# Kernel optimization log

Measured on AMD Instinct MI355X. Metric: run time of the kernel, lower is better.

Reference implementation:

```python
import jax, jax.numpy as jnp
import numpy as np

L, D, H, B, SX, SY, VS, VT = 6, 1024, 16, 4, 512, 512, 32000, 32000
DK = D // H
FF = 4 * D
EPS = 1e-3          # LayerNorm eps (added to std, not var)
SCALE_EMB = float(np.sqrt(D))
NEG = -1e30         # stands in for -inf; fully-masked rows are zeroed after softmax


def pos_encoding(length, d):
    # tensor2tensor-style sinusoid: [sin | cos] concatenated along channels
    nt = d // 2
    lti = np.log(1e4) / (nt - 1)
    inv = np.exp(np.arange(nt) * -lti)
    st = np.arange(length)[:, None] * inv[None, :]
    return jnp.asarray(np.concatenate([np.sin(st), np.cos(st)], axis=1), jnp.float32)


def layer_norm(z, a, b):
    # faithful to the torch module: uses unbiased std (ddof=1) and divides by (std + eps)
    mu = z.mean(-1, keepdims=True)
    sig = jnp.sqrt(((z - mu) ** 2).sum(-1, keepdims=True) / (z.shape[-1] - 1))
    return (z - mu) / (sig + EPS) * a + b


def mha(xq, xkv, wq, wk, wv, wo, mask):
    # xq: (b, lq, D), xkv: (b, lk, D); head-chunking of channel dim == reshape to (H, DK)
    b, lq, _ = xq.shape
    q = (xq @ wq.T).reshape(b, lq, H, DK)
    k = (xkv @ wk.T).reshape(b, -1, H, DK)
    v = (xkv @ wv.T).reshape(b, -1, H, DK)
    s = jnp.einsum('bqhd,bkhd->bhqk', q, k) * (1.0 / np.sqrt(DK))
    m = mask[:, None, :, :]
    s = jnp.where(m, s, NEG)
    att = jax.nn.softmax(s, axis=-1)
    att = att * m.any(-1, keepdims=True)  # replicates NaN->0 for fully masked rows
    c = jnp.einsum('bhqk,bkhd->bqhd', att, v).reshape(b, lq, D)
    return c @ wo.T


def setup_inputs():
    key = jax.random.key(0)
    ks = jax.random.split(key, 10)
    s = 0.02
    emb_x = (jax.random.normal(ks[0], (VS, D), jnp.float32) * s).at[0].set(0.0)  # padding_idx=0
    emb_y = (jax.random.normal(ks[1], (VT, D), jnp.float32) * s).at[0].set(0.0)
    return {
        'emb_x': emb_x, 'emb_y': emb_y,
        'enc_qkvo': jax.random.normal(ks[2], (L, 4, D, D), jnp.float32) * s,
        'enc_ln_s': jnp.ones((L, 2, D), jnp.float32), 'enc_ln_b': jnp.zeros((L, 2, D), jnp.float32),
        'enc_w1': jax.random.normal(ks[3], (L, FF, D), jnp.float32) * s, 'enc_b1': jnp.zeros((L, FF), jnp.float32),
        'enc_w2': jax.random.normal(ks[4], (L, D, FF), jnp.float32) * s, 'enc_b2': jnp.zeros((L, D), jnp.float32),
        'dec_qkvo': jax.random.normal(ks[5], (L, 8, D, D), jnp.float32) * s,
        'dec_ln_s': jnp.ones((L, 3, D), jnp.float32), 'dec_ln_b': jnp.zeros((L, 3, D), jnp.float32),
        'dec_w1': jax.random.normal(ks[6], (L, FF, D), jnp.float32) * s, 'dec_b1': jnp.zeros((L, FF), jnp.float32),
        'dec_w2': jax.random.normal(ks[7], (L, D, FF), jnp.float32) * s, 'dec_b2': jnp.zeros((L, D), jnp.float32),
        'x_block': jax.random.randint(ks[8], (B, SX), 0, VS),
        'y_block': jax.random.randint(ks[9], (B, SY), 0, VT),
    }


def reference(emb_x, emb_y, enc_qkvo, enc_ln_s, enc_ln_b, enc_w1, enc_b1, enc_w2, enc_b2,
              dec_qkvo, dec_ln_s, dec_ln_b, dec_w1, dec_b1, dec_w2, dec_b2, x_block, y_block):
    # internal layout (b, len, D); torch code uses (b, D, len) -- math is identical
    ex = emb_x[x_block] * SCALE_EMB + pos_encoding(SX, D)[None]
    ey = emb_y[y_block] * SCALE_EMB + pos_encoding(SY, D)[None]
    xv = x_block != 0
    yv = y_block != 0
    xx = xv[:, :, None] & xv[:, None, :]                                   # (B, qx, kx)
    xy = yv[:, :, None] & xv[:, None, :]                                   # (B, qy, kx)
    yy = (yv[:, :, None] & yv[:, None, :]) & jnp.tril(jnp.ones((SY, SY), bool))[None]
    e = ex
    for i in range(L):
        sub = mha(e, e, enc_qkvo[i, 0], enc_qkvo[i, 1], enc_qkvo[i, 2], enc_qkvo[i, 3], xx)
        e = layer_norm(e + sub, enc_ln_s[i, 0], enc_ln_b[i, 0])
        sub = jax.nn.relu(e @ enc_w1[i].T + enc_b1[i]) @ enc_w2[i].T + enc_b2[i]
        e = layer_norm(e + sub, enc_ln_s[i, 1], enc_ln_b[i, 1])
    z = e
    e = ey
    for i in range(L):
        sub = mha(e, e, dec_qkvo[i, 0], dec_qkvo[i, 1], dec_qkvo[i, 2], dec_qkvo[i, 3], yy)
        e = layer_norm(e + sub, dec_ln_s[i, 0], dec_ln_b[i, 0])
        sub = mha(e, z, dec_qkvo[i, 4], dec_qkvo[i, 5], dec_qkvo[i, 6], dec_qkvo[i, 7], xy)
        e = layer_norm(e + sub, dec_ln_s[i, 1], dec_ln_b[i, 1])
        sub = jax.nn.relu(e @ dec_w1[i].T + dec_b1[i]) @ dec_w2[i].T + dec_b2[i]
        e = layer_norm(e + sub, dec_ln_s[i, 2], dec_ln_b[i, 2])
    return e @ emb_y.T  # tied output projection -> (B, SY, VT)
```

## Files before the change

### kernel.cpp

```cpp
#include <hip/hip_runtime.h>

typedef unsigned short u16;
typedef float f32x4 __attribute__((ext_vector_type(4)));
typedef __bf16 bf16x8 __attribute__((ext_vector_type(8)));
typedef u16 u16x8 __attribute__((ext_vector_type(8)));

#define DEV __device__ __forceinline__

DEV u16 f2bf(float f) {
  unsigned u = __builtin_bit_cast(unsigned, f);
  u += 0x7fffu + ((u >> 16) & 1u);
  return (u16)(u >> 16);
}

DEV float wsum(float v) {
#pragma unroll
  for (int o = 32; o > 0; o >>= 1) v += __shfl_xor(v, o, 64);
  return v;
}
DEV float gmax16(float v) {
#pragma unroll
  for (int o = 8; o > 0; o >>= 1) v = fmaxf(v, __shfl_xor(v, o, 64));
  return v;
}
DEV float gsum16(float v) {
#pragma unroll
  for (int o = 8; o > 0; o >>= 1) v += __shfl_xor(v, o, 64);
  return v;
}

DEV void gld16(const void* g, void* l) {
  __builtin_amdgcn_global_load_lds((const __attribute__((address_space(1))) void*)g,
                                   (__attribute__((address_space(3))) void*)l, 16, 0, 0);
}

DEV void remap_bxy(int& bx, int& by) {
  const int gx = gridDim.x, gy = gridDim.y;
  const int flat = blockIdx.y * gx + blockIdx.x;
  const int nwg = gx * gy;
  const int q = nwg >> 3, r = nwg & 7;
  const int xcd = flat & 7, li = flat >> 3;
  const int wg = (xcd < r ? xcd * (q + 1) : r * (q + 1) + (xcd - r) * q) + li;
  by = wg % gy;
  bx = wg / gy;
}

template <int BM, int BN, int MODE>
__global__ __launch_bounds__(256, 2) void gemm_k(
    const u16* __restrict__ A, const u16* __restrict__ B, int lda, int ldb, int K,
    float alpha, const float* __restrict__ bias, float* __restrict__ Cf, int ldc,
    u16* __restrict__ Cb, u16* __restrict__ qp, u16* __restrict__ kp,
    u16* __restrict__ vp, int n_off) {
  constexpr int FM = BM / 32, FN = BN / 32;
  constexpr int CHA = BM / 8, CHT = (BM + BN) / 8;
  __shared__ u16 lds[2][(BM + BN) * 64];
  const int lane = threadIdx.x & 63, wid = threadIdx.x >> 6;
  const int wr = wid >> 1, wc = wid & 1;
  int bx, by;
  remap_bxy(bx, by);
  const u16* gA = A + (long)(by * BM) * lda;
  const u16* gB = B + (long)(bx * BN) * ldb;

  const f32x4 zero4 = {0.f, 0.f, 0.f, 0.f};
  f32x4 acc[FM][FN];
#pragma unroll
  for (int m = 0; m < FM; ++m)
#pragma unroll
    for (int n = 0; n < FN; ++n) acc[m][n] = zero4;

  const int r8 = lane >> 3, sl = lane & 7;

  auto stage = [&](int buf, int kt) {
    const int kb = kt << 6;
#pragma unroll
    for (int c0 = 0; c0 < CHT; c0 += 4) {
      const int c = c0 + wid;
      u16* l = &lds[buf][c << 9];
      const u16* g;
      if (c < CHA) {
        int r = (c << 3) + r8;
        g = gA + (long)r * lda + kb + ((sl ^ (r & 7)) << 3);
      } else {
        int r = ((c - CHA) << 3) + r8;
        g = gB + (long)r * ldb + kb + ((sl ^ (r & 7)) << 3);
      }
      gld16(g, l);
    }
  };

  const int KT = K >> 6;
  stage(0, 0);
  __syncthreads();
  int cur = 0;
  for (int kt = 0; kt < KT; ++kt) {
    if (kt + 1 < KT) stage(cur ^ 1, kt + 1);
    const u16* lA = &lds[cur][0];
    const u16* lB = &lds[cur][BM << 6];
#pragma unroll
    for (int kk = 0; kk < 2; ++kk) {
      bf16x8 af[FM], bv[FN];
#pragma unroll
      for (int m = 0; m < FM; ++m) {
        int r = wr * (BM / 2) + m * 16 + (lane & 15);
        int slot = ((kk << 2) | (lane >> 4)) ^ (r & 7);
        af[m] = *(const bf16x8*)(lA + (r << 6) + (slot << 3));
      }
#pragma unroll
      for (int n = 0; n < FN; ++n) {
        int r = wc * (BN / 2) + n * 16 + (lane & 15);
        int slot = ((kk << 2) | (lane >> 4)) ^ (r & 7);
        bv[n] = *(const bf16x8*)(lB + (r << 6) + (slot << 3));
      }
#pragma unroll
      for (int m = 0; m < FM; ++m)
#pragma unroll
        for (int n = 0; n < FN; ++n)
          acc[m][n] = __builtin_amdgcn_mfma_f32_16x16x32_bf16(af[m], bv[n], acc[m][n], 0, 0, 0);
    }
    __syncthreads();
    cur ^= 1;
  }

  const int rb = by * BM + wr * (BM / 2) + ((lane >> 4) << 2);
  const int cb = bx * BN + wc * (BN / 2) + (lane & 15);
#pragma unroll
  for (int m = 0; m < FM; ++m) {
#pragma unroll
    for (int n = 0; n < FN; ++n) {
#pragma unroll
      for (int j = 0; j < 4; ++j) {
        const int row = rb + m * 16 + j;
        const int col = cb + n * 16;
        float v = acc[m][n][j];
        if constexpr (MODE == 0) {
          float r = v * alpha;
          if (bias) r += bias[col];
          Cf[(long)row * ldc + col] = r;
        } else if constexpr (MODE == 1) {
          Cb[(long)row * ldc + col] = f2bf(fmaxf(v + bias[col], 0.f));
        } else {
          int np = col + n_off;
          int sel = np >> 10;
          int dim = np & 1023;
          long base = (((long)(row >> 9) * 16 + (dim >> 6)) * 512 + (row & 511)) * 64 + (dim & 63);
          u16 val = f2bf(v);
          if (sel == 0) qp[base] = val;
          else if (sel == 1) kp[base] = val;
          else vp[base] = val;
        }
      }
    }
  }
}

template <int CAUSAL>
__global__ __launch_bounds__(256, 2) void fattn_k(
    const u16* __restrict__ Qg, const u16* __restrict__ Kg, const u16* __restrict__ Vtg,
    const int* __restrict__ qids, const int* __restrict__ kids, u16* __restrict__ ctx) {
  __shared__ u16 Qs[128 * 64];
  __shared__ u16 Ks[2][64 * 64];
  __shared__ u16 Vs[2][64 * 64];
  __shared__ u16 Ps[4][32 * 64];
  const int lane = threadIdx.x & 63, wid = threadIdx.x >> 6;
  const int qt = blockIdx.x, bh = blockIdx.y, b = bh >> 4, h = bh & 15;
  const int q0 = qt << 7;
  const u16* Qbase = Qg + ((long)bh * 512 + q0) * 64;
  const u16* Kbase = Kg + (long)bh * 512 * 64;
  const u16* Vbase = Vtg + (long)bh * 64 * 512;
  const int r8 = lane >> 3, sl = lane & 7;

#pragma unroll
  for (int c0 = 0; c0 < 16; c0 += 4) {
    int c = c0 + wid;
    int r = (c << 3) + r8;
    gld16(Qbase + (long)r * 64 + ((sl ^ (r & 7)) << 3), &Qs[c << 9]);
  }

  auto stageKV = [&](int buf, int kt) {
#pragma unroll
    for (int c0 = 0; c0 < 16; c0 += 4) {
      int c = c0 + wid;
      if (c < 8) {
        int r = (c << 3) + r8;
        gld16(Kbase + (long)(kt * 64 + r) * 64 + ((sl ^ (r & 7)) << 3), &Ks[buf][c << 9]);
      } else {
        int r = ((c - 8) << 3) + r8;
        gld16(Vbase + (long)r * 512 + kt * 64 + ((sl ^ (r & 7)) << 3), &Vs[buf][(c - 8) << 9]);
      }
    }
  };

  const int NKT = CAUSAL ? ((q0 >> 6) + 2) : 8;
  stageKV(0, 0);
  __syncthreads();

  const f32x4 z4 = {0.f, 0.f, 0.f, 0.f};
  f32x4 oacc[2][4];
  float mrun[2][4], lrun[2][4];
  bool qv[2][4];
#pragma unroll
  for (int m = 0; m < 2; ++m)
#pragma unroll
    for (int j = 0; j < 4; ++j) {
      mrun[m][j] = -3e38f;
      lrun[m][j] = 0.f;
      int qg = q0 + wid * 32 + m * 16 + ((lane >> 4) << 2) + j;
      qv[m][j] = qids[(b << 9) + qg] != 0;
#pragma unroll
      for (int nd = 0; nd < 4; ++nd) oacc[m][nd] = z4;
    }

  int cur = 0;
  for (int kt = 0; kt < NKT; ++kt) {
    if (kt + 1 < NKT) stageKV(cur ^ 1, kt + 1);
    f32x4 s[2][4];
#pragma unroll
    for (int m = 0; m < 2; ++m)
#pragma unroll
      for (int n = 0; n < 4; ++n) s[m][n] = z4;
#pragma unroll
    for (int kk = 0; kk < 2; ++kk) {
      bf16x8 aq[2], bk[4];
#pragma unroll
      for (int m = 0; m < 2; ++m) {
        int r = wid * 32 + m * 16 + (lane & 15);
        int slot = ((kk << 2) | (lane >> 4)) ^ (r & 7);
        aq[m] = *(const bf16x8*)&Qs[(r << 6) + (slot << 3)];
      }
#pragma unroll
      for (int n = 0; n < 4; ++n) {
        int c = n * 16 + (lane & 15);
        int slot = ((kk << 2) | (lane >> 4)) ^ (c & 7);
        bk[n] = *(const bf16x8*)&Ks[cur][(c << 6) + (slot << 3)];
      }
#pragma unroll
      for (int m = 0; m < 2; ++m)
#pragma unroll
        for (int n = 0; n < 4; ++n)
          s[m][n] = __builtin_amdgcn_mfma_f32_16x16x32_bf16(aq[m], bk[n], s[m][n], 0, 0, 0);
    }
    bool kvld[4];
#pragma unroll
    for (int n = 0; n < 4; ++n)
      kvld[n] = kids[(b << 9) + (kt << 6) + (n << 4) + (lane & 15)] != 0;
    float mx[2][4];
#pragma unroll
    for (int m = 0; m < 2; ++m)
#pragma unroll
      for (int j = 0; j < 4; ++j) {
        mx[m][j] = -3e38f;
        int qg = q0 + wid * 32 + m * 16 + ((lane >> 4) << 2) + j;
#pragma unroll
        for (int n = 0; n < 4; ++n) {
          int colg = (kt << 6) + (n << 4) + (lane & 15);
          bool ok = qv[m][j] && kvld[n] && (!CAUSAL || colg <= qg);
          float sv = ok ? s[m][n][j] * 0.125f : -3e38f;
          s[m][n][j] = sv;
          mx[m][j] = fmaxf(mx[m][j], sv);
        }
        mx[m][j] = gmax16(mx[m][j]);
      }
#pragma unroll
    for (int m = 0; m < 2; ++m)
#pragma unroll
      for (int j = 0; j < 4; ++j) {
        float mn = fmaxf(mrun[m][j], mx[m][j]);
        float f = __expf(mrun[m][j] - mn);
        mrun[m][j] = mn;
        float ps = 0.f;
#pragma unroll
        for (int n = 0; n < 4; ++n) {
          float sv = s[m][n][j];
          float p = (sv > -1e37f) ? __expf(sv - mn) : 0.f;
          s[m][n][j] = p;
          ps += p;
        }
        ps = gsum16(ps);
        lrun[m][j] = lrun[m][j] * f + ps;
#pragma unroll
        for (int nd = 0; nd < 4; ++nd) oacc[m][nd][j] *= f;
      }
#pragma unroll
    for (int m = 0; m < 2; ++m)
#pragma unroll
      for (int n = 0; n < 4; ++n)
#pragma unroll
        for (int j = 0; j < 4; ++j) {
          int rl = (m << 4) + ((lane >> 4) << 2) + j;
          int slot = ((n << 1) | ((lane >> 3) & 1)) ^ (rl & 7);
          Ps[wid][(rl << 6) + (slot << 3) + (lane & 7)] = f2bf(s[m][n][j]);
        }
#pragma unroll
    for (int kk = 0; kk < 2; ++kk) {
      bf16x8 pa[2], vv[4];
#pragma unroll
      for (int m = 0; m < 2; ++m) {
        int r = (m << 4) + (lane & 15);
        int slot = ((kk << 2) | (lane >> 4)) ^ (r & 7);
        pa[m] = *(const bf16x8*)&Ps[wid][(r << 6) + (slot << 3)];
      }
#pragma unroll
      for (int nd = 0; nd < 4; ++nd) {
        int rv = (nd << 4) + (lane & 15);
        int slot = ((kk << 2) | (lane >> 4)) ^ (rv & 7);
        vv[nd] = *(const bf16x8*)&Vs[cur][(rv << 6) + (slot << 3)];
      }
#pragma unroll
      for (int m = 0; m < 2; ++m)
#pragma unroll
        for (int nd = 0; nd < 4; ++nd)
          oacc[m][nd] = __builtin_amdgcn_mfma_f32_16x16x32_bf16(pa[m], vv[nd], oacc[m][nd], 0, 0, 0);
    }
    __syncthreads();
    cur ^= 1;
  }
#pragma unroll
  for (int m = 0; m < 2; ++m)
#pragma unroll
    for (int j = 0; j < 4; ++j) {
      float inv = (lrun[m][j] > 0.f) ? 1.0f / lrun[m][j] : 0.f;
      int qg = q0 + wid * 32 + m * 16 + ((lane >> 4) << 2) + j;
      long rowb = (((long)(b << 9) + qg) * 16 + h) * 64;
#pragma unroll
      for (int nd = 0; nd < 4; ++nd) {
        int d = (nd << 4) + (lane & 15);
        ctx[rowb + d] = f2bf(oacc[m][nd][j] * inv);
      }
    }
}

__global__ __launch_bounds__(256) void embed_k(const int* __restrict__ ids,
                                               const float* __restrict__ emb,
                                               float* __restrict__ xo, u16* __restrict__ bfo) {
  const int tok = blockIdx.x, t = threadIdx.x;
  const int s = tok & 511;
  const long id = ids[tok];
  const int d = t * 4;
  float4 ev = *(const float4*)(emb + id * 1024 + d);
  float o[4] = {ev.x * 32.f, ev.y * 32.f, ev.z * 32.f, ev.w * 32.f};
#pragma unroll
  for (int j = 0; j < 4; ++j) {
    int dd = d + j, di = dd & 511;
    float ang = (float)s * expf(-(float)di * 0.0180241494559220821f);
    o[j] += (dd < 512) ? sinf(ang) : cosf(ang);
  }
  *(float4*)(xo + (long)tok * 1024 + d) = make_float4(o[0], o[1], o[2], o[3]);
  ushort4 ob = {f2bf(o[0]), f2bf(o[1]), f2bf(o[2]), f2bf(o[3])};
  *(ushort4*)(bfo + (long)tok * 1024 + d) = ob;
}

__global__ __launch_bounds__(256) void ln_k(const float* __restrict__ x,
                                            const float* __restrict__ sub,
                                            const float* __restrict__ gam,
                                            const float* __restrict__ bet,
                                            float* __restrict__ xo, u16* __restrict__ bfo) {
  __shared__ float red[8];
  const int row = blockIdx.x, t = threadIdx.x;
  const float4 xv = *(const float4*)(x + (long)row * 1024 + t * 4);
  const float4 sv = *(const float4*)(sub + (long)row * 1024 + t * 4);
  float v0 = xv.x + sv.x, v1 = xv.y + sv.y, v2 = xv.z + sv.z, v3 = xv.w + sv.w;
  float sm = wsum(v0 + v1 + v2 + v3);
  if ((t & 63) == 0) red[t >> 6] = sm;
  __syncthreads();
  const float mu = (red[0] + red[1] + red[2] + red[3]) * (1.0f / 1024.0f);
  const float d0 = v0 - mu, d1 = v1 - mu, d2 = v2 - mu, d3 = v3 - mu;
  float ss = wsum(d0 * d0 + d1 * d1 + d2 * d2 + d3 * d3);
  if ((t & 63) == 0) red[4 + (t >> 6)] = ss;
  __syncthreads();
  const float sig = sqrtf((red[4] + red[5] + red[6] + red[7]) * (1.0f / 1023.0f));
  const float inv = 1.0f / (sig + 0.001f);
  const float4 g4 = *(const float4*)(gam + t * 4);
  const float4 b4 = *(const float4*)(bet + t * 4);
  const float o0 = d0 * inv * g4.x + b4.x, o1 = d1 * inv * g4.y + b4.y;
  const float o2 = d2 * inv * g4.z + b4.z, o3 = d3 * inv * g4.w + b4.w;
  *(float4*)(xo + (long)row * 1024 + t * 4) = make_float4(o0, o1, o2, o3);
  ushort4 ob = {f2bf(o0), f2bf(o1), f2bf(o2), f2bf(o3)};
  *(ushort4*)(bfo + (long)row * 1024 + t * 4) = ob;
}

__global__ __launch_bounds__(256) void transpose_v_k(const u16* __restrict__ v,
                                                     u16* __restrict__ vt) {
  __shared__ u16 t[64][72];
  const int bh = blockIdx.y, s0 = blockIdx.x << 6, tid = threadIdx.x;
  const u16* src = v + ((long)bh * 512 + s0) * 64;
  for (int c = tid; c < 512; c += 256) {
    int s = c >> 3, ch = c & 7;
    u16x8 d = *(const u16x8*)(src + s * 64 + ch * 8);
#pragma unroll
    for (int e = 0; e < 8; ++e) t[s][ch * 8 + e] = d[e];
  }
  __syncthreads();
  u16* dst = vt + ((long)bh * 64) * 512 + s0;
  for (int c = tid; c < 512; c += 256) {
    int dk = c >> 3, sc = (c & 7) << 3;
    u16x8 o;
#pragma unroll
    for (int e = 0; e < 8; ++e) o[e] = t[sc + e][dk];
    *(u16x8*)(dst + (long)dk * 512 + sc) = o;
  }
}

__global__ void cvt_k(const float* __restrict__ src, u16* __restrict__ dst, int n4) {
  for (int i = blockIdx.x * 256 + threadIdx.x; i < n4; i += gridDim.x * 256) {
    float4 v = ((const float4*)src)[i];
    ushort4 o = {f2bf(v.x), f2bf(v.y), f2bf(v.z), f2bf(v.w)};
    ((ushort4*)dst)[i] = o;
  }
}

__global__ void cvt3_k(const float* __restrict__ s0, int n0, const float* __restrict__ s1,
                       int n1, const float* __restrict__ s2, int n2, u16* __restrict__ dst) {
  const int tot = n0 + n1 + n2;
  for (int i = blockIdx.x * 256 + threadIdx.x; i < tot; i += gridDim.x * 256) {
    const float* s;
    int j;
    if (i < n0) { s = s0; j = i; }
    else if (i < n0 + n1) { s = s1; j = i - n0; }
    else { s = s2; j = i - n0 - n1; }
    float4 v = ((const float4*)s)[j];
    ushort4 o = {f2bf(v.x), f2bf(v.y), f2bf(v.z), f2bf(v.w)};
    ((ushort4*)dst)[i] = o;
  }
}

extern "C" void kernel_launch(void* const* d_in, const int* in_sizes, int n_in, void* d_out,
                              int out_size, void* d_ws, size_t ws_size, hipStream_t stream) {
  (void)in_sizes; (void)n_in; (void)out_size;
  const float* emb_x = (const float*)d_in[0];
  const float* emb_y = (const float*)d_in[1];
  const float* enc_qkvo = (const float*)d_in[2];
  const float* enc_ln_s = (const float*)d_in[3];
  const float* enc_ln_b = (const float*)d_in[4];
  const float* enc_w1 = (const float*)d_in[5];
  const float* enc_b1 = (const float*)d_in[6];
  const float* enc_w2 = (const float*)d_in[7];
  const float* enc_b2 = (const float*)d_in[8];
  const float* dec_qkvo = (const float*)d_in[9];
  const float* dec_ln_s = (const float*)d_in[10];
  const float* dec_ln_b = (const float*)d_in[11];
  const float* dec_w1 = (const float*)d_in[12];
  const float* dec_b1 = (const float*)d_in[13];
  const float* dec_w2 = (const float*)d_in[14];
  const float* dec_b2 = (const float*)d_in[15];
  const int* x_block = (const int*)d_in[16];
  const int* y_block = (const int*)d_in[17];

  const long TOK = 2048, Dm = 1024, M1 = 1048576;
  char* p = (char*)d_ws;
  auto alloc = [&](long bytes) { char* r = p; p += (bytes + 255) & ~255L; return r; };
  float* e32 = (float*)alloc(TOK * Dm * 4);
  float* sub = (float*)alloc(TOK * Dm * 4);
  u16* ebf = (u16*)alloc(TOK * Dm * 2);
  u16* zbf = (u16*)alloc(TOK * Dm * 2);
  u16* qb = (u16*)alloc(TOK * Dm * 2);
  u16* kb = (u16*)alloc(TOK * Dm * 2);
  u16* vb = (u16*)alloc(TOK * Dm * 2);
  u16* vtb = (u16*)alloc(TOK * Dm * 2);
  u16* ctx = (u16*)alloc(TOK * Dm * 2);
  u16* hbuf = (u16*)alloc(TOK * 4096 * 2);
  u16* wbuf = (u16*)alloc(16L * M1 * 2);
  u16* embyb = (u16*)alloc(32000L * 1024 * 2);
  if ((size_t)(p - (char*)d_ws) > ws_size) return;

  auto gemmF = [&](const u16* A, const u16* Bw, int M, int N, int K, int lda, int ldb,
                   float alpha, const float* bias, float* C, int ldc) {
    if (N % 128 == 0 && N > 1024) {
      dim3 g(N / 128, M / 128);
      gemm_k<128, 128, 0><<<g, 256, 0, stream>>>(A, Bw, lda, ldb, K, alpha, bias, C, ldc,
                                                 nullptr, nullptr, nullptr, nullptr, 0);
    } else {
      dim3 g(N / 64, M / 128);
      gemm_k<128, 64, 0><<<g, 256, 0, stream>>>(A, Bw, lda, ldb, K, alpha, bias, C, ldc,
                                                nullptr, nullptr, nullptr, nullptr, 0);
    }
  };
  auto gemmRelu = [&](const u16* A, const u16* Bw, const float* bias, u16* C) {
    dim3 g(32, 16);
    gemm_k<128, 128, 1><<<g, 256, 0, stream>>>(A, Bw, 1024, 1024, 1024, 1.f, bias, nullptr,
                                               4096, C, nullptr, nullptr, nullptr, 0);
  };
  auto gemmQKV = [&](const u16* A, const u16* Bw, int N, int n_off) {
    if (N >= 2048) {
      dim3 g(N / 128, 16);
      gemm_k<128, 128, 2><<<g, 256, 0, stream>>>(A, Bw, 1024, 1024, 1024, 1.f, nullptr,
                                                 nullptr, 0, nullptr, qb, kb, vb, n_off);
    } else {
      dim3 g(N / 64, 16);
      gemm_k<128, 64, 2><<<g, 256, 0, stream>>>(A, Bw, 1024, 1024, 1024, 1.f, nullptr,
                                                nullptr, 0, nullptr, qb, kb, vb, n_off);
    }
  };
  auto attn = [&](const int* qids, const int* kids, int causal) {
    transpose_v_k<<<dim3(8, 64), 256, 0, stream>>>(vb, vtb);
    if (causal)
      fattn_k<1><<<dim3(4, 64), 256, 0, stream>>>(qb, kb, vtb, qids, kids, ctx);
    else
      fattn_k<0><<<dim3(4, 64), 256, 0, stream>>>(qb, kb, vtb, qids, kids, ctx);
  };
  auto lnorm = [&](const float* g, const float* b) {
    ln_k<<<2048, 256, 0, stream>>>(e32, sub, g, b, e32, ebf);
  };

  cvt_k<<<2048, 256, 0, stream>>>(emb_y, embyb, 32000 * 1024 / 4);

  embed_k<<<2048, 256, 0, stream>>>(x_block, emb_x, e32, ebf);
  for (int i = 0; i < 6; ++i) {
    cvt3_k<<<2048, 256, 0, stream>>>(enc_qkvo + (long)i * 4 * M1, (int)M1,
                                     enc_w1 + (long)i * 4 * M1, (int)M1,
                                     enc_w2 + (long)i * 4 * M1, (int)M1, wbuf);
    gemmQKV(ebf, wbuf, 3072, 0);
    attn(x_block, x_block, 0);
    gemmF(ctx, wbuf + 3L * M1, 2048, 1024, 1024, 1024, 1024, 1.f, nullptr, sub, 1024);
    lnorm(enc_ln_s + (i * 2 + 0) * 1024, enc_ln_b + (i * 2 + 0) * 1024);
    gemmRelu(ebf, wbuf + 4L * M1, enc_b1 + i * 4096, hbuf);
    gemmF(hbuf, wbuf + 8L * M1, 2048, 1024, 4096, 4096, 4096, 1.f, enc_b2 + i * 1024, sub, 1024);
    lnorm(enc_ln_s + (i * 2 + 1) * 1024, enc_ln_b + (i * 2 + 1) * 1024);
  }
  hipMemcpyAsync(zbf, ebf, TOK * Dm * 2, hipMemcpyDeviceToDevice, stream);

  embed_k<<<2048, 256, 0, stream>>>(y_block, emb_y, e32, ebf);
  for (int i = 0; i < 6; ++i) {
    cvt3_k<<<2048, 256, 0, stream>>>(dec_qkvo + (long)i * 8 * M1, (int)(2 * M1),
                                     dec_w1 + (long)i * 4 * M1, (int)M1,
                                     dec_w2 + (long)i * 4 * M1, (int)M1, wbuf);
    gemmQKV(ebf, wbuf, 3072, 0);
    attn(y_block, y_block, 1);
    gemmF(ctx, wbuf + 3L * M1, 2048, 1024, 1024, 1024, 1024, 1.f, nullptr, sub, 1024);
    lnorm(dec_ln_s + (i * 3 + 0) * 1024, dec_ln_b + (i * 3 + 0) * 1024);
    gemmQKV(ebf, wbuf + 4L * M1, 1024, 0);
    gemmQKV(zbf, wbuf + 5L * M1, 2048, 1024);
    attn(y_block, x_block, 0);
    gemmF(ctx, wbuf + 7L * M1, 2048, 1024, 1024, 1024, 1024, 1.f, nullptr, sub, 1024);
    lnorm(dec_ln_s + (i * 3 + 1) * 1024, dec_ln_b + (i * 3 + 1) * 1024);
    gemmRelu(ebf, wbuf + 8L * M1, dec_b1 + i * 4096, hbuf);
    gemmF(hbuf, wbuf + 12L * M1, 2048, 1024, 4096, 4096, 4096, 1.f, dec_b2 + i * 1024, sub, 1024);
    lnorm(dec_ln_s + (i * 3 + 2) * 1024, dec_ln_b + (i * 3 + 2) * 1024);
  }
  gemmF(ebf, embyb, 2048, 32000, 1024, 1024, 1024, 1.f, nullptr, (float*)d_out, 32000);
}
```

Baseline: 2.655 ms.

## Deepen GEMM LDS pipeline, fuse V transpose into QKV epilogue, prioritize attention MFMAs

The GEMM main loop now uses a 4-deep ring of K=32 LDS stages with explicit vmcnt waits and a single barrier per step, where before it double-buffered K=64 tiles. This is meant to hide global-load latency better. The QKV GEMM epilogue now writes V directly in transposed layout through an LDS staging tile, which removes the separate transpose kernel and the extra V buffer. The attention kernel raises wave priority around its MFMA blocks. The risks are more barriers per K, since the steps are half as deep, and correctness of the hand-written waitcnt counts.

```diff
diff --git a/kernel.cpp b/kernel.cpp
--- a/kernel.cpp
+++ b/kernel.cpp
@@ -32,6 +32,15 @@
 DEV void gld16(const void* g, void* l) {
   __builtin_amdgcn_global_load_lds((const __attribute__((address_space(1))) void*)g,
                                    (__attribute__((address_space(3))) void*)l, 16, 0, 0);
+}
+
+template <int N>
+DEV void vwait() {
+  if constexpr (N == 0) asm volatile("s_waitcnt vmcnt(0)" ::: "memory");
+  else if constexpr (N == 3) asm volatile("s_waitcnt vmcnt(3)" ::: "memory");
+  else if constexpr (N == 4) asm volatile("s_waitcnt vmcnt(4)" ::: "memory");
+  else if constexpr (N == 6) asm volatile("s_waitcnt vmcnt(6)" ::: "memory");
+  else asm volatile("s_waitcnt vmcnt(8)" ::: "memory");
 }
 
 DEV void remap_bxy(int& bx, int& by) {
@@ -52,8 +61,8 @@
     u16* __restrict__ Cb, u16* __restrict__ qp, u16* __restrict__ kp,
     u16* __restrict__ vp, int n_off) {
   constexpr int FM = BM / 32, FN = BN / 32;
-  constexpr int CHA = BM / 8, CHT = (BM + BN) / 8;
-  __shared__ u16 lds[2][(BM + BN) * 64];
+  constexpr int R = (BM + BN) >> 6;
+  __shared__ u16 lds[4][(BM + BN) * 32];
   const int lane = threadIdx.x & 63, wid = threadIdx.x >> 6;
   const int wr = wid >> 1, wc = wid & 1;
   int bx, by;
@@ -68,88 +77,121 @@
 #pragma unroll
     for (int n = 0; n < FN; ++n) acc[m][n] = zero4;
 
-  const int r8 = lane >> 3, sl = lane & 7;
-
-  auto stage = [&](int buf, int kt) {
-    const int kb = kt << 6;
-#pragma unroll
-    for (int c0 = 0; c0 < CHT; c0 += 4) {
-      const int c = c0 + wid;
-      u16* l = &lds[buf][c << 9];
-      const u16* g;
-      if (c < CHA) {
-        int r = (c << 3) + r8;
-        g = gA + (long)r * lda + kb + ((sl ^ (r & 7)) << 3);
-      } else {
-        int r = ((c - CHA) << 3) + r8;
-        g = gB + (long)r * ldb + kb + ((sl ^ (r & 7)) << 3);
-      }
-      gld16(g, l);
-    }
-  };
-
-  const int KT = K >> 6;
-  stage(0, 0);
-  __syncthreads();
-  int cur = 0;
-  for (int kt = 0; kt < KT; ++kt) {
-    if (kt + 1 < KT) stage(cur ^ 1, kt + 1);
-    const u16* lA = &lds[cur][0];
-    const u16* lB = &lds[cur][BM << 6];
-#pragma unroll
-    for (int kk = 0; kk < 2; ++kk) {
-      bf16x8 af[FM], bv[FN];
-#pragma unroll
-      for (int m = 0; m < FM; ++m) {
-        int r = wr * (BM / 2) + m * 16 + (lane & 15);
-        int slot = ((kk << 2) | (lane >> 4)) ^ (r & 7);
-        af[m] = *(const bf16x8*)(lA + (r << 6) + (slot << 3));
-      }
-#pragma unroll
-      for (int n = 0; n < FN; ++n) {
-        int r = wc * (BN / 2) + n * 16 + (lane & 15);
-        int slot = ((kk << 2) | (lane >> 4)) ^ (r & 7);
-        bv[n] = *(const bf16x8*)(lB + (r << 6) + (slot << 3));
-      }
-#pragma unroll
-      for (int m = 0; m < FM; ++m)
-#pragma unroll
-        for (int n = 0; n < FN; ++n)
-          acc[m][n] = __builtin_amdgcn_mfma_f32_16x16x32_bf16(af[m], bv[n], acc[m][n], 0, 0, 0);
-    }
-    __syncthreads();
-    cur ^= 1;
+  auto stage = [&](int t) {
+    const int kb = t << 5;
+    u16* lbase = &lds[t & 3][0];
+#pragma unroll
+    for (int rd = 0; rd < R; ++rd) {
+      const int c = rd * 256 + threadIdx.x;
+      const int r = c >> 2;
+      const int sg = (c & 3) ^ ((r >> 1) & 3);
+      const u16* g = (r < BM) ? (gA + (long)r * lda + kb + (sg << 3))
+                              : (gB + (long)(r - BM) * ldb + kb + (sg << 3));
+      gld16(g, lbase + (c << 3));
+    }
+  };
+
+  const int KT = K >> 5;
+  stage(0);
+  stage(1);
+  stage(2);
+  for (int t = 0; t < KT; ++t) {
+    const int rem = KT - 1 - t;
+    if (rem >= 2) vwait<2 * R>();
+    else if (rem == 1) vwait<R>();
+    else vwait<0>();
+    __builtin_amdgcn_s_barrier();
+    __builtin_amdgcn_sched_barrier(0);
+    if (t + 3 < KT) stage(t + 3);
+    const u16* lA = &lds[t & 3][0];
+    const u16* lB = lA + (BM << 5);
+    bf16x8 af[FM], bv[FN];
+#pragma unroll
+    for (int m = 0; m < FM; ++m) {
+      int r = wr * (BM / 2) + m * 16 + (lane & 15);
+      int sg = (lane >> 4) ^ ((r >> 1) & 3);
+      af[m] = *(const bf16x8*)(lA + (r << 5) + (sg << 3));
+    }
+#pragma unroll
+    for (int n = 0; n < FN; ++n) {
+      int c = wc * (BN / 2) + n * 16 + (lane & 15);
+      int sg = (lane >> 4) ^ ((c >> 1) & 3);
+      bv[n] = *(const bf16x8*)(lB + (c << 5) + (sg << 3));
+    }
+#pragma unroll
+    for (int m = 0; m < FM; ++m)
+#pragma unroll
+      for (int n = 0; n < FN; ++n)
+        acc[m][n] = __builtin_amdgcn_mfma_f32_16x16x32_bf16(af[m], bv[n], acc[m][n], 0, 0, 0);
+    __builtin_amdgcn_sched_barrier(0);
   }
 
   const int rb = by * BM + wr * (BM / 2) + ((lane >> 4) << 2);
   const int cb = bx * BN + wc * (BN / 2) + (lane & 15);
-#pragma unroll
-  for (int m = 0; m < FM; ++m) {
-#pragma unroll
-    for (int n = 0; n < FN; ++n) {
-#pragma unroll
-      for (int j = 0; j < 4; ++j) {
-        const int row = rb + m * 16 + j;
-        const int col = cb + n * 16;
-        float v = acc[m][n][j];
-        if constexpr (MODE == 0) {
-          float r = v * alpha;
-          if (bias) r += bias[col];
-          Cf[(long)row * ldc + col] = r;
-        } else if constexpr (MODE == 1) {
-          Cb[(long)row * ldc + col] = f2bf(fmaxf(v + bias[col], 0.f));
-        } else {
-          int np = col + n_off;
-          int sel = np >> 10;
-          int dim = np & 1023;
-          long base = (((long)(row >> 9) * 16 + (dim >> 6)) * 512 + (row & 511)) * 64 + (dim & 63);
-          u16 val = f2bf(v);
-          if (sel == 0) qp[base] = val;
-          else if (sel == 1) kp[base] = val;
-          else vp[base] = val;
+  if constexpr (MODE == 2) {
+    const bool isV = (bx * BN + n_off) >= 2048;
+    if (isV) {
+      __syncthreads();
+      u16* T = (u16*)&lds[0][0];
+      constexpr int TS = BM + 8;
+#pragma unroll
+      for (int m = 0; m < FM; ++m)
+#pragma unroll
+        for (int n = 0; n < FN; ++n) {
+          int cl = wc * (BN / 2) + n * 16 + (lane & 15);
+#pragma unroll
+          for (int j = 0; j < 4; ++j) {
+            int rl = wr * (BM / 2) + m * 16 + ((lane >> 4) << 2) + j;
+            T[cl * TS + rl] = f2bf(acc[m][n][j]);
+          }
         }
-      }
-    }
+      __syncthreads();
+      const int vcb = bx * BN + n_off - 2048;
+      const int b = (by * BM) >> 9, s0 = (by * BM) & 511;
+#pragma unroll
+      for (int p = 0; p < BM * BN / 2048; ++p) {
+        int idx = p * 2048 + threadIdx.x * 8;
+        int dl = idx / BM, sl = idx & (BM - 1);
+        u16x8 o;
+#pragma unroll
+        for (int e = 0; e < 8; ++e) o[e] = T[dl * TS + sl + e];
+        int vc = vcb + dl;
+        *(u16x8*)(vp + (((long)b * 16 + (vc >> 6)) * 64 + (vc & 63)) * 512 + s0 + sl) = o;
+      }
+    } else {
+#pragma unroll
+      for (int m = 0; m < FM; ++m)
+#pragma unroll
+        for (int n = 0; n < FN; ++n)
+#pragma unroll
+          for (int j = 0; j < 4; ++j) {
+            const int row = rb + m * 16 + j;
+            const int np = cb + n * 16 + n_off;
+            const int sel = np >> 10, dim = np & 1023;
+            long base = (((long)(row >> 9) * 16 + (dim >> 6)) * 512 + (row & 511)) * 64 + (dim & 63);
+            u16 val = f2bf(acc[m][n][j]);
+            if (sel == 0) qp[base] = val;
+            else kp[base] = val;
+          }
+    }
+  } else {
+#pragma unroll
+    for (int m = 0; m < FM; ++m)
+#pragma unroll
+      for (int n = 0; n < FN; ++n)
+#pragma unroll
+        for (int j = 0; j < 4; ++j) {
+          const int row = rb + m * 16 + j;
+          const int col = cb + n * 16;
+          float v = acc[m][n][j];
+          if constexpr (MODE == 0) {
+            float r = v * alpha;
+            if (bias) r += bias[col];
+            Cf[(long)row * ldc + col] = r;
+          } else {
+            Cb[(long)row * ldc + col] = f2bf(fmaxf(v + bias[col], 0.f));
+          }
+        }
   }
 }
 
@@ -218,6 +260,7 @@
     for (int m = 0; m < 2; ++m)
 #pragma unroll
       for (int n = 0; n < 4; ++n) s[m][n] = z4;
+    __builtin_amdgcn_s_setprio(1);
 #pragma unroll
     for (int kk = 0; kk < 2; ++kk) {
       bf16x8 aq[2], bk[4];
@@ -239,6 +282,7 @@
         for (int n = 0; n < 4; ++n)
           s[m][n] = __builtin_amdgcn_mfma_f32_16x16x32_bf16(aq[m], bk[n], s[m][n], 0, 0, 0);
     }
+    __builtin_amdgcn_s_setprio(0);
     bool kvld[4];
 #pragma unroll
     for (int n = 0; n < 4; ++n)
@@ -290,6 +334,7 @@
           int slot = ((n << 1) | ((lane >> 3) & 1)) ^ (rl & 7);
           Ps[wid][(rl << 6) + (slot << 3) + (lane & 7)] = f2bf(s[m][n][j]);
         }
+    __builtin_amdgcn_s_setprio(1);
 #pragma unroll
     for (int kk = 0; kk < 2; ++kk) {
       bf16x8 pa[2], vv[4];
@@ -311,6 +356,7 @@
         for (int nd = 0; nd < 4; ++nd)
           oacc[m][nd] = __builtin_amdgcn_mfma_f32_16x16x32_bf16(pa[m], vv[nd], oacc[m][nd], 0, 0, 0);
     }
+    __builtin_amdgcn_s_setprio(0);
     __syncthreads();
     cur ^= 1;
   }
@@ -378,28 +424,6 @@
   *(ushort4*)(bfo + (long)row * 1024 + t * 4) = ob;
 }
 
-__global__ __launch_bounds__(256) void transpose_v_k(const u16* __restrict__ v,
-                                                     u16* __restrict__ vt) {
-  __shared__ u16 t[64][72];
-  const int bh = blockIdx.y, s0 = blockIdx.x << 6, tid = threadIdx.x;
-  const u16* src = v + ((long)bh * 512 + s0) * 64;
-  for (int c = tid; c < 512; c += 256) {
-    int s = c >> 3, ch = c & 7;
-    u16x8 d = *(const u16x8*)(src + s * 64 + ch * 8);
-#pragma unroll
-    for (int e = 0; e < 8; ++e) t[s][ch * 8 + e] = d[e];
-  }
-  __syncthreads();
-  u16* dst = vt + ((long)bh * 64) * 512 + s0;
-  for (int c = tid; c < 512; c += 256) {
-    int dk = c >> 3, sc = (c & 7) << 3;
-    u16x8 o;
-#pragma unroll
-    for (int e = 0; e < 8; ++e) o[e] = t[sc + e][dk];
-    *(u16x8*)(dst + (long)dk * 512 + sc) = o;
-  }
-}
-
 __global__ void cvt_k(const float* __restrict__ src, u16* __restrict__ dst, int n4) {
   for (int i = blockIdx.x * 256 + threadIdx.x; i < n4; i += gridDim.x * 256) {
     float4 v = ((const float4*)src)[i];
@@ -454,7 +478,6 @@
   u16* zbf = (u16*)alloc(TOK * Dm * 2);
   u16* qb = (u16*)alloc(TOK * Dm * 2);
   u16* kb = (u16*)alloc(TOK * Dm * 2);
-  u16* vb = (u16*)alloc(TOK * Dm * 2);
   u16* vtb = (u16*)alloc(TOK * Dm * 2);
   u16* ctx = (u16*)alloc(TOK * Dm * 2);
   u16* hbuf = (u16*)alloc(TOK * 4096 * 2);
@@ -483,15 +506,14 @@
     if (N >= 2048) {
       dim3 g(N / 128, 16);
       gemm_k<128, 128, 2><<<g, 256, 0, stream>>>(A, Bw, 1024, 1024, 1024, 1.f, nullptr,
-                                                 nullptr, 0, nullptr, qb, kb, vb, n_off);
+                                                 nullptr, 0, nullptr, qb, kb, vtb, n_off);
     } else {
       dim3 g(N / 64, 16);
       gemm_k<128, 64, 2><<<g, 256, 0, stream>>>(A, Bw, 1024, 1024, 1024, 1.f, nullptr,
-                                                nullptr, 0, nullptr, qb, kb, vb, n_off);
+                                                nullptr, 0, nullptr, qb, kb, vtb, n_off);
     }
   };
   auto attn = [&](const int* qids, const int* kids, int causal) {
-    transpose_v_k<<<dim3(8, 64), 256, 0, stream>>>(vb, vtb);
     if (causal)
       fattn_k<1><<<dim3(4, 64), 256, 0, stream>>>(qb, kb, vtb, qids, kids, ctx);
     else
```

New measurement: 2.547 ms. -4.1%, faster.
